# Optimization experiments

Hardware: AMD Instinct MI355X
Metric: run time of the kernel (lower is better)

## Reference

```python
import jax, jax.numpy as jnp
import numpy as np

NUM_CLASSES = 8
NUM_MAPS = 4
FEAT_C = 2048  # ResNet-50 layer4 channels
HW = 14        # spatial size (448/32)


def setup_inputs() -> dict:
    key = jax.random.key(0)
    k1, k2, k3, k4, k5 = jax.random.split(key, 5)
    B = 64
    x = jax.random.normal(k1, (B, FEAT_C, HW, HW), dtype=jnp.float32)
    down_w = jax.random.normal(k2, (NUM_CLASSES * NUM_MAPS, FEAT_C), dtype=jnp.float32) * 0.02
    down_b = jax.random.normal(k3, (NUM_CLASSES * NUM_MAPS,), dtype=jnp.float32) * 0.02
    fc_w = jax.random.normal(k4, (NUM_CLASSES, 2 * FEAT_C), dtype=jnp.float32) * 0.02
    fc_b = jax.random.normal(k5, (NUM_CLASSES,), dtype=jnp.float32) * 0.02
    return {"x": x, "down_w": down_w, "down_b": down_b, "fc_w": fc_w, "fc_b": fc_b}


def reference(x, down_w, down_b, fc_w, fc_b):
    B = x.shape[0]
    x_ori = x  # [B, 2048, 14, 14] (ResNet features output)
    # downconv: 1x1 conv 2048 -> num_classes*num_maps
    xc = jnp.einsum('bchw,oc->bohw', x_ori, down_w) + down_b[None, :, None, None]  # [B,32,14,14]
    # GMP over full 14x14 window -> [B, 32]
    gmp = jnp.max(xc, axis=(2, 3))
    # spatial_pooling = ClassWisePool(num_maps): mean over groups of num_maps channels
    scores = gmp.reshape(B, NUM_CLASSES, NUM_MAPS).mean(axis=2)  # [B, 8]
    x_out = jax.nn.log_softmax(scores, axis=1)  # first output
    # class-wise pool on the full conv map: [B,32,14,14] -> [B,8,14,14]
    xcp = xc.reshape(B, NUM_CLASSES, NUM_MAPS, HW, HW).mean(axis=2)
    # modulate each class map by its (log-softmax) score
    xcp = xcp * x_out[:, :, None, None]
    # spatial_pooling2 = ClassWisePool(num_classes): mean over 8 class channels -> [B,1,14,14]
    sal = xcp.mean(axis=1, keepdims=True)
    prod = sal * x_ori  # [B,2048,14,14] via broadcast (fused, no copies)
    cat = jnp.concatenate([x_ori, prod], axis=1)  # [B,4096,14,14]
    # GAP 14x14 -> [B,4096]
    gap = cat.mean(axis=(2, 3))
    logits2 = gap @ fc_w.T + fc_b  # [B,8]
    x_conv_out = jax.nn.log_softmax(logits2, axis=1)
    return (x_out, x_conv_out)
```

## Files before the change

### kernel.cpp

```cpp
#include <hip/hip_runtime.h>

#define NCH 2048
#define HW 196
#define NB 64
#define NOUT 48
#define NCHUNK 8
#define CPC (NCH / NCHUNK)
#define KS_PER_BLK (CPC / 32)
#define KGTOT (NCH / 32)
#define NT 13
#define MT 3
#define TILE_F (32 * HW)
#define TILE_V4 (TILE_F / 4)

typedef __attribute__((ext_vector_type(8))) short bf16x8;
typedef __attribute__((ext_vector_type(4))) float f32x4;

__device__ __forceinline__ short f2bf(float f) {
    unsigned int u = __float_as_uint(f);
    u = u + 0x7fffu + ((u >> 16) & 1u);
    return (short)(u >> 16);
}

__global__ void build_afrag(const float* __restrict__ down_w,
                            const float* __restrict__ fc_w,
                            bf16x8* __restrict__ afrag) {
    int t = blockIdx.x * 256 + threadIdx.x;
    if (t >= KGTOT * MT * 64) return;
    int lane = t & 63;
    int frag = t >> 6;
    int mt = frag % MT;
    int kg = frag / MT;
    int o = mt * 16 + (lane & 15);
    int cbase = kg * 32 + (lane >> 4) * 8;
    bf16x8 v;
#pragma unroll
    for (int j = 0; j < 8; ++j) {
        int c = cbase + j;
        float w;
        if (o < 32)      w = down_w[o * NCH + c];
        else if (o < 40) w = fc_w[(o - 32) * (2 * NCH) + NCH + c];
        else             w = fc_w[(o - 40) * (2 * NCH) + c];
        v[j] = f2bf(w);
    }
    afrag[frag * 64 + lane] = v;
}

__global__ __launch_bounds__(256) void conv_mfma(const float* __restrict__ x,
                                                 const bf16x8* __restrict__ afrag,
                                                 float* __restrict__ part) {
    __shared__ float ldsx[2][TILE_F];
    const int chunk = blockIdx.x;
    const int b = blockIdx.y;
    const int tid = threadIdx.x;
    const int wave = tid >> 6;
    const int lane = tid & 63;
    const int nsub = lane & 15;
    const int kq = lane >> 4;

    f32x4 acc[4][MT];
#pragma unroll
    for (int i = 0; i < 4; ++i)
#pragma unroll
        for (int m = 0; m < MT; ++m)
            acc[i][m] = (f32x4){0.f, 0.f, 0.f, 0.f};

    int pidx[4];
#pragma unroll
    for (int i = 0; i < 4; ++i) {
        int p = (wave + 4 * i) * 16 + nsub;
        pidx[i] = (p < HW) ? p : (HW - 1);
    }

    const float* xtile0 = x + ((size_t)b * NCH + (size_t)chunk * CPC) * HW;

    auto stage = [&](int ks, int bb) {
        const float* g = xtile0 + (size_t)ks * TILE_F;
#pragma unroll
        for (int r = 0; r < 7; ++r) {
            int q = r * 256 + tid;
            if (q < TILE_V4) {
                __builtin_amdgcn_global_load_lds(
                    (const __attribute__((address_space(1))) unsigned int*)(g + (size_t)q * 4),
                    (__attribute__((address_space(3))) unsigned int*)(&ldsx[bb][(r * 256 + wave * 64) * 4]),
                    16, 0, 0);
            }
        }
    };

    stage(0, 0);

    for (int ks = 0; ks < KS_PER_BLK; ++ks) {
        __syncthreads();
        if (ks + 1 < KS_PER_BLK) stage(ks + 1, (ks + 1) & 1);

        const int kg = chunk * KS_PER_BLK + ks;
        bf16x8 a0 = afrag[(kg * MT + 0) * 64 + lane];
        bf16x8 a1 = afrag[(kg * MT + 1) * 64 + lane];
        bf16x8 a2 = afrag[(kg * MT + 2) * 64 + lane];

        const float* base = &ldsx[ks & 1][kq * 8 * HW];
#pragma unroll
        for (int i = 0; i < 4; ++i) {
            const float* bp = base + pidx[i];
            float f[8];
#pragma unroll
            for (int j = 0; j < 8; ++j) f[j] = bp[j * HW];
            bf16x8 bv;
#pragma unroll
            for (int j = 0; j < 8; ++j) bv[j] = f2bf(f[j]);
            acc[i][0] = __builtin_amdgcn_mfma_f32_16x16x32_bf16(a0, bv, acc[i][0], 0, 0, 0);
            acc[i][1] = __builtin_amdgcn_mfma_f32_16x16x32_bf16(a1, bv, acc[i][1], 0, 0, 0);
            acc[i][2] = __builtin_amdgcn_mfma_f32_16x16x32_bf16(a2, bv, acc[i][2], 0, 0, 0);
        }
    }

    float* pb = part + (size_t)(b * NCHUNK + chunk) * (NT * NOUT * 16);
#pragma unroll
    for (int i = 0; i < 4; ++i) {
        int nt = wave + 4 * i;
        if (nt < NT) {
            float* d = pb + nt * (NOUT * 16) + kq * 64 + nsub;
#pragma unroll
            for (int m = 0; m < MT; ++m)
#pragma unroll
                for (int r = 0; r < 4; ++r)
                    d[m * 256 + r * 16] = acc[i][m][r];
        }
    }
}

__global__ __launch_bounds__(256) void reduce_part(const float* __restrict__ part,
                                                   float* __restrict__ T) {
    int idx = blockIdx.x * 256 + threadIdx.x;
    if (idx >= NB * NOUT * HW) return;
    int b = idx / (NOUT * HW);
    int rem = idx - b * (NOUT * HW);
    int o = rem / HW;
    int p = rem - o * HW;
    int nt = p >> 4, ns = p & 15;
    const float* src = part + (size_t)b * NCHUNK * NT * NOUT * 16
                     + nt * (NOUT * 16) + o * 16 + ns;
    float s = 0.f;
#pragma unroll
    for (int ch = 0; ch < NCHUNK; ++ch)
        s += src[(size_t)ch * NT * NOUT * 16];
    T[idx] = s;
}

__global__ __launch_bounds__(256) void finish(const float* __restrict__ T,
                                              const float* __restrict__ down_b,
                                              const float* __restrict__ fc_b,
                                              float* __restrict__ out) {
    const int b = blockIdx.x;
    const int tid = threadIdx.x;
    __shared__ float Ts[NOUT * HW];
    __shared__ float gmpS[32];
    __shared__ float scoreS[8];
    __shared__ float xoS[8];
    __shared__ float salS[HW];
    __shared__ float logitS[8];

    {
        const float4* src = (const float4*)(T + (size_t)b * NOUT * HW);
        float4* dst = (float4*)Ts;
        for (int i = tid; i < NOUT * HW / 4; i += 256) dst[i] = src[i];
    }
    __syncthreads();

    if (tid < 32) {
        float m = -1e30f;
        for (int p = 0; p < HW; ++p) m = fmaxf(m, Ts[tid * HW + p]);
        gmpS[tid] = m + down_b[tid];
    }
    __syncthreads();

    if (tid < 8)
        scoreS[tid] = 0.25f * (gmpS[4 * tid] + gmpS[4 * tid + 1] +
                               gmpS[4 * tid + 2] + gmpS[4 * tid + 3]);
    __syncthreads();

    if (tid < 8) {
        float m = -1e30f;
        for (int k = 0; k < 8; ++k) m = fmaxf(m, scoreS[k]);
        float se = 0.f;
        for (int k = 0; k < 8; ++k) se += expf(scoreS[k] - m);
        float xo = scoreS[tid] - m - logf(se);
        xoS[tid] = xo;
        out[b * 8 + tid] = xo;
    }
    __syncthreads();

    if (tid < HW) {
        float s = 0.f;
#pragma unroll
        for (int k = 0; k < 8; ++k) {
            float bs = down_b[4 * k] + down_b[4 * k + 1] +
                       down_b[4 * k + 2] + down_b[4 * k + 3];
            float rs = Ts[(4 * k) * HW + tid] + Ts[(4 * k + 1) * HW + tid] +
                       Ts[(4 * k + 2) * HW + tid] + Ts[(4 * k + 3) * HW + tid] + bs;
            s += xoS[k] * rs;
        }
        salS[tid] = s * (1.f / 32.f);
    }
    __syncthreads();

    if (tid < 8) {
        float t1 = 0.f, t2 = 0.f;
        for (int p = 0; p < HW; ++p) {
            t1 += Ts[(40 + tid) * HW + p];
            t2 += salS[p] * Ts[(32 + tid) * HW + p];
        }
        logitS[tid] = (t1 + t2) * (1.f / 196.f) + fc_b[tid];
    }
    __syncthreads();

    if (tid < 8) {
        float m = -1e30f;
        for (int k = 0; k < 8; ++k) m = fmaxf(m, logitS[k]);
        float se = 0.f;
        for (int k = 0; k < 8; ++k) se += expf(logitS[k] - m);
        out[NB * 8 + b * 8 + tid] = logitS[tid] - m - logf(se);
    }
}

extern "C" void kernel_launch(void* const* d_in, const int* in_sizes, int n_in,
                              void* d_out, int out_size, void* d_ws, size_t ws_size,
                              hipStream_t stream) {
    const float* x      = (const float*)d_in[0];
    const float* down_w = (const float*)d_in[1];
    const float* down_b = (const float*)d_in[2];
    const float* fc_w   = (const float*)d_in[3];
    const float* fc_b   = (const float*)d_in[4];
    float* out = (float*)d_out;

    bf16x8* afrag = (bf16x8*)d_ws;
    float* T    = (float*)((char*)d_ws + (size_t)KGTOT * MT * 64 * 16);
    float* part = T + (size_t)NB * NOUT * HW;

    build_afrag<<<(KGTOT * MT * 64 + 255) / 256, 256, 0, stream>>>(down_w, fc_w, afrag);
    conv_mfma<<<dim3(NCHUNK, NB), 256, 0, stream>>>(x, afrag, part);
    reduce_part<<<(NB * NOUT * HW + 255) / 256, 256, 0, stream>>>(part, T);
    finish<<<NB, 256, 0, stream>>>(T, down_b, fc_b, out);
}
```

Measured before the change: 186.2 us.

## Fuse partial-sum reduction into finish kernel and use cheaper bf16 packing

The separate reduce_part kernel is removed. The finish kernel now sums the eight chunk partials straight from the partial buffer into shared memory, which saves one launch and one global round trip through T. Separately, the fp32-to-bf16 conversion in the MFMA inner loop switches from round-to-nearest-even to round-half-up plus a byte permute, which cuts ALU work per element but changes rounding slightly. The finish kernel runs only 64 blocks, so the reduction now has less parallelism.

```diff
diff --git a/kernel.cpp b/kernel.cpp
--- a/kernel.cpp
+++ b/kernel.cpp
@@ -12,9 +12,12 @@
 #define MT 3
 #define TILE_F (32 * HW)
 #define TILE_V4 (TILE_F / 4)
+#define SLAB (NT * NOUT * 16)
+#define SLAB4 (SLAB / 4)
 
 typedef __attribute__((ext_vector_type(8))) short bf16x8;
 typedef __attribute__((ext_vector_type(4))) float f32x4;
+typedef __attribute__((ext_vector_type(4))) int i32x4;
 
 __device__ __forceinline__ short f2bf(float f) {
     unsigned int u = __float_as_uint(f);
@@ -103,19 +106,23 @@
 #pragma unroll
         for (int i = 0; i < 4; ++i) {
             const float* bp = base + pidx[i];
-            float f[8];
-#pragma unroll
-            for (int j = 0; j < 8; ++j) f[j] = bp[j * HW];
-            bf16x8 bv;
-#pragma unroll
-            for (int j = 0; j < 8; ++j) bv[j] = f2bf(f[j]);
+            unsigned int u[8];
+#pragma unroll
+            for (int j = 0; j < 8; ++j)
+                u[j] = __float_as_uint(bp[j * HW]) + 0x8000u;
+            i32x4 bi;
+            bi[0] = (int)__builtin_amdgcn_perm(u[1], u[0], 0x07060302u);
+            bi[1] = (int)__builtin_amdgcn_perm(u[3], u[2], 0x07060302u);
+            bi[2] = (int)__builtin_amdgcn_perm(u[5], u[4], 0x07060302u);
+            bi[3] = (int)__builtin_amdgcn_perm(u[7], u[6], 0x07060302u);
+            bf16x8 bv = __builtin_bit_cast(bf16x8, bi);
             acc[i][0] = __builtin_amdgcn_mfma_f32_16x16x32_bf16(a0, bv, acc[i][0], 0, 0, 0);
             acc[i][1] = __builtin_amdgcn_mfma_f32_16x16x32_bf16(a1, bv, acc[i][1], 0, 0, 0);
             acc[i][2] = __builtin_amdgcn_mfma_f32_16x16x32_bf16(a2, bv, acc[i][2], 0, 0, 0);
         }
     }
 
-    float* pb = part + (size_t)(b * NCHUNK + chunk) * (NT * NOUT * 16);
+    float* pb = part + (size_t)(b * NCHUNK + chunk) * SLAB;
 #pragma unroll
     for (int i = 0; i < 4; ++i) {
         int nt = wave + 4 * i;
@@ -130,25 +137,7 @@
     }
 }
 
-__global__ __launch_bounds__(256) void reduce_part(const float* __restrict__ part,
-                                                   float* __restrict__ T) {
-    int idx = blockIdx.x * 256 + threadIdx.x;
-    if (idx >= NB * NOUT * HW) return;
-    int b = idx / (NOUT * HW);
-    int rem = idx - b * (NOUT * HW);
-    int o = rem / HW;
-    int p = rem - o * HW;
-    int nt = p >> 4, ns = p & 15;
-    const float* src = part + (size_t)b * NCHUNK * NT * NOUT * 16
-                     + nt * (NOUT * 16) + o * 16 + ns;
-    float s = 0.f;
-#pragma unroll
-    for (int ch = 0; ch < NCHUNK; ++ch)
-        s += src[(size_t)ch * NT * NOUT * 16];
-    T[idx] = s;
-}
-
-__global__ __launch_bounds__(256) void finish(const float* __restrict__ T,
+__global__ __launch_bounds__(256) void finish(const float* __restrict__ part,
                                               const float* __restrict__ down_b,
                                               const float* __restrict__ fc_b,
                                               float* __restrict__ out) {
@@ -162,9 +151,23 @@
     __shared__ float logitS[8];
 
     {
-        const float4* src = (const float4*)(T + (size_t)b * NOUT * HW);
-        float4* dst = (float4*)Ts;
-        for (int i = tid; i < NOUT * HW / 4; i += 256) dst[i] = src[i];
+        const float4* base = (const float4*)(part + (size_t)b * NCHUNK * SLAB);
+        for (int i4 = tid; i4 < SLAB4; i4 += 256) {
+            float4 s = base[i4];
+#pragma unroll
+            for (int ch = 1; ch < NCHUNK; ++ch) {
+                float4 v = base[(size_t)ch * SLAB4 + i4];
+                s.x += v.x; s.y += v.y; s.z += v.z; s.w += v.w;
+            }
+            int nt = i4 / 192;
+            int rem = i4 - nt * 192;
+            int o = rem >> 2, ns4 = rem & 3;
+            int p = nt * 16 + ns4 * 4;
+            float vv[4] = {s.x, s.y, s.z, s.w};
+#pragma unroll
+            for (int q = 0; q < 4; ++q)
+                if (p + q < HW) Ts[o * HW + p + q] = vv[q];
+        }
     }
     __syncthreads();
 
@@ -235,11 +238,9 @@
     float* out = (float*)d_out;
 
     bf16x8* afrag = (bf16x8*)d_ws;
-    float* T    = (float*)((char*)d_ws + (size_t)KGTOT * MT * 64 * 16);
-    float* part = T + (size_t)NB * NOUT * HW;
+    float* part = (float*)((char*)d_ws + (size_t)KGTOT * MT * 64 * 16);
 
     build_afrag<<<(KGTOT * MT * 64 + 255) / 256, 256, 0, stream>>>(down_w, fc_w, afrag);
     conv_mfma<<<dim3(NCHUNK, NB), 256, 0, stream>>>(x, afrag, part);
-    reduce_part<<<(NB * NOUT * HW + 255) / 256, 256, 0, stream>>>(part, T);
-    finish<<<NB, 256, 0, stream>>>(T, down_b, fc_b, out);
-}
+    finish<<<NB, 256, 0, stream>>>(part, down_b, fc_b, out);
+}
```

Measured after the change: 183.3 us. About the same (-1.5%).
